# Performance work log

Measured on AMD Instinct MI355X. Metric: run time of the kernel, lower is better.

Reference implementation:

```python
import math
import jax, jax.numpy as jnp
import numpy as np

B, T, DIN, DH, E, TOPK = 2048, 512, 32, 96, 6, 2


def setup_inputs() -> dict:
    key = jax.random.key(0)
    ks = jax.random.split(key, 20)
    x = jax.random.normal(ks[0], (B, T, DIN), jnp.float32)
    lengths = jax.random.randint(ks[1], (B,), 1, T + 1)
    mask = (jnp.arange(T)[None, :] < lengths[:, None])

    def U(k, shape, fan):
        s = 1.0 / math.sqrt(fan)
        return jax.random.uniform(k, shape, jnp.float32, -s, s)

    # PyTorch LSTM init: U(-1/sqrt(DH), 1/sqrt(DH)); gate order i,f,g,o
    Wih = U(ks[2], (4 * DH, DIN), DH)
    Whh = U(ks[3], (4 * DH, DH), DH)
    bih = U(ks[4], (4 * DH,), DH)
    bhh = U(ks[5], (4 * DH,), DH)
    Wq = U(ks[6], (DH, DH), DH); bq = U(ks[7], (DH,), DH)
    Wk = U(ks[8], (DH, DH), DH); bk = U(ks[9], (DH,), DH)
    Wv = U(ks[10], (DH, DH), DH); bv = U(ks[11], (DH,), DH)
    Wg = U(ks[12], (E, 2 * DH), 2 * DH); bg = U(ks[13], (E,), 2 * DH)
    We1 = U(ks[14], (E, DH, 2 * DH), 2 * DH); be1 = U(ks[15], (E, DH), 2 * DH)
    We2 = U(ks[16], (E, DH), DH); be2 = U(ks[17], (E,), DH)
    return dict(x=x, lengths=lengths, mask=mask, Wih=Wih, Whh=Whh, bih=bih, bhh=bhh,
                Wq=Wq, bq=bq, Wk=Wk, bk=bk, Wv=Wv, bv=bv, Wg=Wg, bg=bg,
                We1=We1, be1=be1, We2=We2, be2=be2)


def _lstm(x, mask, Wih, Whh, bih, bhh):
    # packed-sequence semantics: carry frozen past each sample's length,
    # padded output positions zeroed (like pad_packed_sequence).
    xg = x @ Wih.T + bih  # [B,T,4*DH] precomputed input projection
    dh = Whh.shape[1]

    def step(carry, inp):
        h, c = carry
        xg_t, m_t = inp
        g = xg_t + h @ Whh.T + bhh
        i, f, gg, o = jnp.split(g, 4, axis=-1)
        c_new = jax.nn.sigmoid(f) * c + jax.nn.sigmoid(i) * jnp.tanh(gg)
        h_new = jax.nn.sigmoid(o) * jnp.tanh(c_new)
        m = m_t[:, None]
        h = jnp.where(m, h_new, h)
        c = jnp.where(m, c_new, c)
        return (h, c), jnp.where(m, h_new, 0.0)

    init = (jnp.zeros((x.shape[0], dh), x.dtype), jnp.zeros((x.shape[0], dh), x.dtype))
    (hT, _), H = jax.lax.scan(step, init, (jnp.swapaxes(xg, 0, 1), mask.T))
    return jnp.swapaxes(H, 0, 1), hT  # H:[B,T,DH], hT:[B,DH]


def reference(x, lengths, mask, Wih, Whh, bih, bhh, Wq, bq, Wk, bk, Wv, bv,
              Wg, bg, We1, be1, We2, be2):
    H, hT = _lstm(x, mask, Wih, Whh, bih, bhh)
    Q = hT @ Wq.T + bq                      # [B,DH]
    K = H @ Wk.T + bk                       # [B,T,DH]
    V = H @ Wv.T + bv                       # [B,T,DH]
    logits = jnp.einsum('bd,btd->bt', Q, K) / math.sqrt(K.shape[-1])
    logits = jnp.where(mask, logits, -1e9)
    alpha = jax.nn.softmax(logits, axis=1)  # [B,T]
    ctx = jnp.einsum('bt,btd->bd', alpha, V)
    feats = jnp.concatenate([ctx, hT], axis=-1)  # [B,2*DH]
    gate_logits = feats @ Wg.T + bg              # [B,E]
    topv, topi = jax.lax.top_k(gate_logits, TOPK)
    pi = jax.nn.softmax(topv, axis=-1)           # [B,TOPK]
    # all-expert dense compute (E tiny), then gather selected -> same math as
    # the per-expert masked scatter loop in the torch module (dropout off).
    h1 = jax.nn.relu(jnp.einsum('bf,ehf->beh', feats, We1) + be1[None])  # [B,E,DH]
    outs = jnp.einsum('beh,eh->be', h1, We2) + be2[None]                  # [B,E]
    sel = jnp.take_along_axis(outs, topi, axis=1)                         # [B,TOPK]
    yhat = jnp.sum(pi * sel, axis=-1, keepdims=True)                      # [B,1]
    return yhat, alpha, gate_logits
```

## Files before the change

kernel.cpp:

```cpp
#include <hip/hip_runtime.h>
#include <hip/hip_bf16.h>

#define B_ 2048
#define T_ 512
#define DIN_ 32
#define DH_ 96
#define NG_ 384
#define E_ 6

#define BPB 8
#define HP 104
#define GS 10

typedef __attribute__((ext_vector_type(8))) _Float16 f16x8;
typedef __attribute__((ext_vector_type(4))) float f32x4;

#if defined(__has_builtin)
# if __has_builtin(__builtin_amdgcn_exp2f)
#  define EXP2F(x) __builtin_amdgcn_exp2f(x)
# endif
# if __has_builtin(__builtin_amdgcn_rcpf)
#  define RCPF(x) __builtin_amdgcn_rcpf(x)
# endif
#endif
#ifndef EXP2F
# define EXP2F(x) exp2f(x)
#endif
#ifndef RCPF
# define RCPF(x) (1.0f/(x))
#endif

__device__ __forceinline__ float sigf(float x) {
    return RCPF(1.0f + EXP2F(x * -1.44269504f));
}
__device__ __forceinline__ float tanhf_(float x) {
    return 1.0f - 2.0f * RCPF(1.0f + EXP2F(x * 2.88539008f));
}

__device__ __forceinline__ f16x8 cvt8(float4 a, float4 b) {
    f16x8 r;
    r[0] = (_Float16)a.x; r[1] = (_Float16)a.y; r[2] = (_Float16)a.z; r[3] = (_Float16)a.w;
    r[4] = (_Float16)b.x; r[5] = (_Float16)b.y; r[6] = (_Float16)b.z; r[7] = (_Float16)b.w;
    return r;
}
__device__ __forceinline__ f16x8 cvt8p(const float* p) {
    return cvt8(*(const float4*)p, *(const float4*)(p + 4));
}

__device__ __forceinline__ void lds_barrier() {
    asm volatile("s_waitcnt lgkmcnt(0)\n\ts_barrier" ::: "memory");
}

__global__ __launch_bounds__(512) void sort_kernel(
    const int* __restrict__ lengths, int* __restrict__ perm) {
    __shared__ int sbins[512];
    __shared__ int soffs[512];
    const int tid = threadIdx.x;
    sbins[tid] = 0;
    __syncthreads();
    for (int b = tid; b < B_; b += 512) atomicAdd(&sbins[lengths[b] - 1], 1);
    __syncthreads();
    soffs[tid] = sbins[tid];
    __syncthreads();
    for (int d = 1; d < 512; d <<= 1) {
        int v = (tid >= d) ? soffs[tid - d] : 0;
        __syncthreads();
        soffs[tid] += v;
        __syncthreads();
    }
    int excl = soffs[tid] - sbins[tid];
    __syncthreads();
    soffs[tid] = excl;
    __syncthreads();
    for (int b = tid; b < B_; b += 512) {
        const int pos = atomicAdd(&soffs[lengths[b] - 1], 1);
        perm[pos] = b;
    }
}

__global__ __launch_bounds__(768, 1) void lstm_attn_kernel(
    const float* __restrict__ x, const int* __restrict__ lengths,
    const int* __restrict__ perm,
    const float* __restrict__ Wih, const float* __restrict__ Whh,
    const float* __restrict__ bih, const float* __restrict__ bhh,
    const float* __restrict__ Wq, const float* __restrict__ bq,
    const float* __restrict__ Wk, const float* __restrict__ bk,
    const float* __restrict__ Wv, const float* __restrict__ bv,
    const float* __restrict__ Wg, const float* __restrict__ bg,
    const float* __restrict__ We1, const float* __restrict__ be1,
    const float* __restrict__ We2, const float* __restrict__ be2,
    _Float16* __restrict__ Hout,
    float* __restrict__ yhat_out, float* __restrict__ alpha_out,
    float* __restrict__ gl_out)
{
    __shared__ float sgate[NG_ * GS];
    __shared__ _Float16 sh[2][8 * HP];
    __shared__ int sgb[BPB], slen[BPB];
    __shared__ float slog[BPB][T_];
    __shared__ float shT8[BPB][DH_];
    __shared__ float sQ8[BPB][DH_];
    __shared__ float sqk8[BPB][DH_];
    __shared__ float scraw[BPB][DH_];
    __shared__ float sfeats[BPB][2 * DH_];
    __shared__ float sh1_[BPB][2][DH_];
    __shared__ float sqb[BPB];
    __shared__ float sgl[BPB][E_];
    __shared__ float spi2[BPB][2];
    __shared__ float souts[BPB][2];
    __shared__ int stopi2[BPB][2];

    const int tid  = threadIdx.x;
    const int bb   = blockIdx.x * BPB;
    const int wave = tid >> 6;
    const int lane = tid & 63;
    const int col  = lane & 15;
    const int quad = lane >> 4;

    if (tid < BPB) {
        const int g = perm[bb + tid];
        sgb[tid] = g;
        slen[tid] = lengths[g];
    }
    {
        _Float16* shf = &sh[0][0];
        for (int i = tid; i < 2 * 8 * HP; i += 768) shf[i] = (_Float16)0.f;
    }
    __syncthreads();

    int bmax = slen[0];
#pragma unroll
    for (int i = 1; i < BPB; ++i) bmax = max(bmax, slen[i]);

    int gc[2]; float bias[2];
    f16x8 wh[2][3], wi[2];
#pragma unroll
    for (int j = 0; j < 2; ++j) {
        const int tau = wave * 2 + j;
        const int g = tau / 6, u6 = tau % 6;
        const int gcj = g * DH_ + u6 * 16 + col;
        gc[j] = gcj;
#pragma unroll
        for (int kf = 0; kf < 3; ++kf)
            wh[j][kf] = cvt8p(Whh + gcj * DH_ + kf * 32 + quad * 8);
        wi[j] = cvt8p(Wih + gcj * DIN_ + quad * 8);
        bias[j] = bih[gcj] + bhh[gcj];
    }

    const int eu = tid >> 3;
    const int eb = tid & 7;
    float c1 = 0.f, hk1 = 0.f;
    const int len1 = slen[eb];

    const bool st_act = tid < 384;
    const int sb = tid / 48;
    const int su = (tid % 48) * 2;
    _Float16* Hst = Hout + ((long long)sgb[sb] * T_) * DH_ + su;

    const bool arow = col < 8;
    const float* xp = x + ((long long)sgb[col & 7] * T_) * DIN_ + quad * 8;
    float4 xc0 = make_float4(0.f, 0.f, 0.f, 0.f), xc1 = xc0;
    if (arow) { xc0 = *(const float4*)xp; xc1 = *(const float4*)(xp + 4); }

    for (int t = 0; t < bmax; ++t) {
        const int buf = t & 1;

        f16x8 h0 = 0, h1 = 0, h2 = 0;
        if (arow) {
            const _Float16* hrow = &sh[buf][col * HP];
            h0 = *(const f16x8*)(hrow + 0  + quad * 8);
            h1 = *(const f16x8*)(hrow + 32 + quad * 8);
            h2 = *(const f16x8*)(hrow + 64 + quad * 8);
        }

        const float* xpn = (t + 1 < T_) ? (xp + DIN_) : xp;
        float4 xn0 = make_float4(0.f, 0.f, 0.f, 0.f), xn1 = xn0;
        if (arow) { xn0 = *(const float4*)xpn; xn1 = *(const float4*)(xpn + 4); }

        f16x8 xa = cvt8(xc0, xc1);

#pragma unroll
        for (int j = 0; j < 2; ++j) {
            f32x4 a = {bias[j], bias[j], bias[j], bias[j]};
            a = __builtin_amdgcn_mfma_f32_16x16x32_f16(h0, wh[j][0], a, 0, 0, 0);
            a = __builtin_amdgcn_mfma_f32_16x16x32_f16(h1, wh[j][1], a, 0, 0, 0);
            a = __builtin_amdgcn_mfma_f32_16x16x32_f16(h2, wh[j][2], a, 0, 0, 0);
            a = __builtin_amdgcn_mfma_f32_16x16x32_f16(xa, wi[j],    a, 0, 0, 0);
            if (quad < 2) {
                float2* sp = (float2*)&sgate[gc[j] * GS + quad * 4];
                sp[0] = float2{a[0], a[1]};
                sp[1] = float2{a[2], a[3]};
            }
        }
        lds_barrier();

        if (t > 0 && st_act) {
            unsigned v = *(const unsigned*)&sh[buf][sb * HP + su];
            *(unsigned*)Hst = v;
            Hst += DH_;
        }

        {
            float iv = sgate[(0 * DH_ + eu) * GS + eb];
            float fv = sgate[(1 * DH_ + eu) * GS + eb];
            float gv = sgate[(2 * DH_ + eu) * GS + eb];
            float ov = sgate[(3 * DH_ + eu) * GS + eb];
            float cn = sigf(fv) * c1 + sigf(iv) * tanhf_(gv);
            float hn = sigf(ov) * tanhf_(cn);
            const bool m = t < len1;
            c1  = m ? cn : c1;
            hk1 = m ? hn : hk1;
            sh[buf ^ 1][eb * HP + eu] = (_Float16)hk1;
        }
        lds_barrier();

        xp = xpn; xc0 = xn0; xc1 = xn1;
    }

    if (st_act) {
        unsigned v = *(const unsigned*)&sh[bmax & 1][sb * HP + su];
        *(unsigned*)Hst = v;
    }

    shT8[eb][eu] = hk1;
    __threadfence_block();
    __syncthreads();

    const int abi = tid / 96;
    const int au  = tid - abi * 96;
    const int ag  = sgb[abi];
    const int alen = slen[abi];
    const float scale = 0.10206207262f;

    {
        float acc = bq[au];
        const float* wr = Wq + au * DH_;
        const float* ht = &shT8[abi][0];
        for (int d = 0; d < DH_; d += 4) {
            float4 w4 = *(const float4*)(wr + d);
            acc += w4.x * ht[d] + w4.y * ht[d + 1] + w4.z * ht[d + 2] + w4.w * ht[d + 3];
        }
        sQ8[abi][au] = acc;
    }
    __syncthreads();

    {
        float acc = 0.f;
        const float* qv = &sQ8[abi][0];
        for (int j = 0; j < DH_; ++j) acc += Wk[j * DH_ + au] * qv[j];
        sqk8[abi][au] = acc * scale;
    }
    if (wave < 8) {
        float p = sQ8[wave][lane] * bk[lane];
        if (lane < 32) p += sQ8[wave][64 + lane] * bk[64 + lane];
        for (int off = 32; off; off >>= 1) p += __shfl_xor(p, off);
        if (lane == 0) sqb[wave] = p * scale;
    }
    __syncthreads();

    for (int k = 0; k < 6; ++k) {
        const int r = tid + k * 768;
        if (r < BPB * T_) {
            const int bi2 = r >> 9, t = r & (T_ - 1);
            float l = -1e30f;
            if (t < slen[bi2]) {
                const _Float16* hr = Hout + ((long long)sgb[bi2] * T_ + t) * DH_;
                const float* qk = &sqk8[bi2][0];
                float acc = sqb[bi2];
#pragma unroll
                for (int u = 0; u < DH_; u += 8) {
                    f16x8 hv = *(const f16x8*)(hr + u);
                    float4 qa = *(const float4*)(qk + u);
                    float4 qc = *(const float4*)(qk + u + 4);
                    acc += (float)hv[0] * qa.x + (float)hv[1] * qa.y
                         + (float)hv[2] * qa.z + (float)hv[3] * qa.w
                         + (float)hv[4] * qc.x + (float)hv[5] * qc.y
                         + (float)hv[6] * qc.z + (float)hv[7] * qc.w;
                }
                l = acc;
            }
            slog[0][r] = l;
        }
    }
    __syncthreads();

    if (wave < 8) {
        float lv[8];
#pragma unroll
        for (int j = 0; j < 8; ++j) lv[j] = slog[wave][lane + 64 * j];
        float m = lv[0];
#pragma unroll
        for (int j = 1; j < 8; ++j) m = fmaxf(m, lv[j]);
        for (int off = 32; off; off >>= 1) m = fmaxf(m, __shfl_xor(m, off));
        float ev[8]; float s = 0.f;
#pragma unroll
        for (int j = 0; j < 8; ++j) { ev[j] = EXP2F((lv[j] - m) * 1.44269504f); s += ev[j]; }
        for (int off = 32; off; off >>= 1) s += __shfl_xor(s, off);
        const float rinv = RCPF(s);
        float* aout = alpha_out + (long long)sgb[wave] * T_;
#pragma unroll
        for (int j = 0; j < 8; ++j) {
            const float a = ev[j] * rinv;
            slog[wave][lane + 64 * j] = a;
            aout[lane + 64 * j] = a;
        }
    }
    __syncthreads();

    {
        const int ub = au >> 3, tl = au & 7;
        float acc[8] = {0.f, 0.f, 0.f, 0.f, 0.f, 0.f, 0.f, 0.f};
        const _Float16* hb = Hout + ((long long)ag * T_) * DH_ + ub * 8;
        for (int k = 0; k < 64; ++k) {
            const int t = tl + (k << 3);
            if (t < alen) {
                f16x8 hv = *(const f16x8*)(hb + t * DH_);
                const float a = slog[abi][t];
#pragma unroll
                for (int i = 0; i < 8; ++i) acc[i] += a * (float)hv[i];
            }
        }
#pragma unroll
        for (int i = 0; i < 8; ++i) {
            acc[i] += __shfl_xor(acc[i], 1);
            acc[i] += __shfl_xor(acc[i], 2);
            acc[i] += __shfl_xor(acc[i], 4);
        }
        if (tl == 0) {
#pragma unroll
            for (int i = 0; i < 8; ++i) scraw[abi][ub * 8 + i] = acc[i];
        }
    }
    __syncthreads();

    {
        float acc = bv[au];
        const float* wr = Wv + au * DH_;
        const float* cr = &scraw[abi][0];
        for (int u2 = 0; u2 < DH_; u2 += 4) {
            float4 w4 = *(const float4*)(wr + u2);
            acc += w4.x * cr[u2] + w4.y * cr[u2 + 1] + w4.z * cr[u2 + 2] + w4.w * cr[u2 + 3];
        }
        sfeats[abi][au] = acc;
        sfeats[abi][DH_ + au] = shT8[abi][au];
    }
    __syncthreads();

    {
        const int ge = au >> 4, gcc = au & 15;
        float p = 0.f;
        const float* wg = Wg + ge * 2 * DH_ + gcc * 12;
        const float* ft = &sfeats[abi][gcc * 12];
#pragma unroll
        for (int j = 0; j < 12; ++j) p += wg[j] * ft[j];
        p += __shfl_xor(p, 1); p += __shfl_xor(p, 2);
        p += __shfl_xor(p, 4); p += __shfl_xor(p, 8);
        if (gcc == 0) {
            const float g2 = p + bg[ge];
            sgl[abi][ge] = g2;
            gl_out[ag * E_ + ge] = g2;
        }
    }
    __syncthreads();

    if (tid < BPB) {
        int i0 = 0; float v0 = sgl[tid][0];
        for (int ee = 1; ee < E_; ++ee) if (sgl[tid][ee] > v0) { v0 = sgl[tid][ee]; i0 = ee; }
        int i1 = -1; float v1 = -1e30f;
        for (int ee = 0; ee < E_; ++ee) {
            if (ee == i0) continue;
            if (sgl[tid][ee] > v1) { v1 = sgl[tid][ee]; i1 = ee; }
        }
        const float ex1 = EXP2F((v1 - v0) * 1.44269504f);
        const float inv = RCPF(1.f + ex1);
        spi2[tid][0] = inv; spi2[tid][1] = ex1 * inv;
        stopi2[tid][0] = i0; stopi2[tid][1] = i1;
    }
    __syncthreads();

#pragma unroll
    for (int e2 = 0; e2 < 2; ++e2) {
        const int ex = stopi2[abi][e2];
        float acc = be1[ex * DH_ + au];
        const float* w = We1 + ((long long)ex * DH_ + au) * (2 * DH_);
        const float* ft = &sfeats[abi][0];
        for (int f = 0; f < 2 * DH_; f += 4) {
            float4 w4 = *(const float4*)(w + f);
            acc += w4.x * ft[f] + w4.y * ft[f + 1] + w4.z * ft[f + 2] + w4.w * ft[f + 3];
        }
        sh1_[abi][e2][au] = fmaxf(acc, 0.f);
    }
    __syncthreads();

    if (wave < 8) {
        const int e2 = lane >> 5, lu = lane & 31;
        const int ex = stopi2[wave][e2];
        const float* w2 = We2 + ex * DH_;
        const float* h1p = &sh1_[wave][e2][0];
        float p = h1p[lu] * w2[lu] + h1p[lu + 32] * w2[lu + 32] + h1p[lu + 64] * w2[lu + 64];
        p += __shfl_xor(p, 1); p += __shfl_xor(p, 2); p += __shfl_xor(p, 4);
        p += __shfl_xor(p, 8); p += __shfl_xor(p, 16);
        if (lu == 0) souts[wave][e2] = p + be2[ex];
    }
    __syncthreads();
    if (tid < BPB)
        yhat_out[sgb[tid]] = spi2[tid][0] * souts[tid][0] + spi2[tid][1] * souts[tid][1];
}

extern "C" void kernel_launch(void* const* d_in, const int* in_sizes, int n_in,
                              void* d_out, int out_size, void* d_ws, size_t ws_size,
                              hipStream_t stream) {
    const float* x   = (const float*)d_in[0];
    const int* lengths = (const int*)d_in[1];
    const float* Wih = (const float*)d_in[3];
    const float* Whh = (const float*)d_in[4];
    const float* bih = (const float*)d_in[5];
    const float* bhh = (const float*)d_in[6];
    const float* Wq  = (const float*)d_in[7];
    const float* bq  = (const float*)d_in[8];
    const float* Wk  = (const float*)d_in[9];
    const float* bk  = (const float*)d_in[10];
    const float* Wv  = (const float*)d_in[11];
    const float* bv  = (const float*)d_in[12];
    const float* Wg  = (const float*)d_in[13];
    const float* bg  = (const float*)d_in[14];
    const float* We1 = (const float*)d_in[15];
    const float* be1 = (const float*)d_in[16];
    const float* We2 = (const float*)d_in[17];
    const float* be2 = (const float*)d_in[18];

    float* yhat  = (float*)d_out;
    float* alpha = yhat + B_;
    float* gl    = alpha + (size_t)B_ * T_;

    char* ws = (char*)d_ws;
    _Float16* Hws = (_Float16*)ws;
    int* perm   = (int*)(ws + (size_t)B_ * T_ * DH_ * 2);

    sort_kernel<<<dim3(1), dim3(512), 0, stream>>>(lengths, perm);

    lstm_attn_kernel<<<dim3(B_ / BPB), dim3(768), 0, stream>>>(
        x, lengths, perm, Wih, Whh, bih, bhh,
        Wq, bq, Wk, bk, Wv, bv, Wg, bg, We1, be1, We2, be2,
        Hws, yhat, alpha, gl);
}
```

Baseline: 718.6 us.

## Offload attention and MoE tail for long-sequence groups to a separate per-sample kernel

LSTM blocks whose longest sequence exceeds a threshold now write the final hidden state to workspace and exit early, skipping the in-kernel attention and MoE epilogue. A new kernel with one block per sample then does attention, gating and experts for those groups. This shortens the critical-path blocks, which already run the longest recurrences, and spreads their epilogue across many small blocks. The cost is an extra launch, a round trip of hT through global memory, and a re-read of H.

```diff
diff --git a/kernel.cpp b/kernel.cpp
--- a/kernel.cpp
+++ b/kernel.cpp
@@ -11,6 +11,7 @@
 #define BPB 8
 #define HP 104
 #define GS 10
+#define ATH 384
 
 typedef __attribute__((ext_vector_type(8))) _Float16 f16x8;
 typedef __attribute__((ext_vector_type(4))) float f32x4;
@@ -89,7 +90,7 @@
     const float* __restrict__ Wg, const float* __restrict__ bg,
     const float* __restrict__ We1, const float* __restrict__ be1,
     const float* __restrict__ We2, const float* __restrict__ be2,
-    _Float16* __restrict__ Hout,
+    _Float16* __restrict__ Hout, float* __restrict__ hT,
     float* __restrict__ yhat_out, float* __restrict__ alpha_out,
     float* __restrict__ gl_out)
 {
@@ -221,6 +222,10 @@
         *(unsigned*)Hst = v;
     }
 
+    hT[sgb[eb] * DH_ + eu] = hk1;
+
+    if (bmax > ATH) return;
+
     shT8[eb][eu] = hk1;
     __threadfence_block();
     __syncthreads();
@@ -404,6 +409,212 @@
     __syncthreads();
     if (tid < BPB)
         yhat_out[sgb[tid]] = spi2[tid][0] * souts[tid][0] + spi2[tid][1] * souts[tid][1];
+}
+
+__global__ __launch_bounds__(256) void attn_moe_kernel(
+    const _Float16* __restrict__ H, const float* __restrict__ hT,
+    const int* __restrict__ lengths, const int* __restrict__ perm,
+    const float* __restrict__ Wq, const float* __restrict__ bq,
+    const float* __restrict__ Wk, const float* __restrict__ bk,
+    const float* __restrict__ Wv, const float* __restrict__ bv,
+    const float* __restrict__ Wg, const float* __restrict__ bg,
+    const float* __restrict__ We1, const float* __restrict__ be1,
+    const float* __restrict__ We2, const float* __restrict__ be2,
+    float* __restrict__ yhat_out, float* __restrict__ alpha_out,
+    float* __restrict__ gl_out)
+{
+    const int p = blockIdx.x;
+    int gbm = 0;
+#pragma unroll
+    for (int k = 0; k < BPB; ++k)
+        gbm = max(gbm, lengths[perm[(p & ~(BPB - 1)) + k]]);
+    if (gbm <= ATH) return;
+
+    __shared__ float salpha[T_];
+    __shared__ float shT[DH_];
+    __shared__ float sQ[DH_];
+    __shared__ float sqk[DH_];
+    __shared__ float spart[DH_];
+    __shared__ float sfeats[2 * DH_];
+    __shared__ float sh1[2][DH_];
+    __shared__ float sred[4], ssum[4];
+    __shared__ float sgl[E_];
+    __shared__ float spi[2];
+    __shared__ float souts[2];
+    __shared__ float sqb_s;
+    __shared__ int stopi[2];
+
+    const int b = perm[p];
+    const int tid = threadIdx.x;
+    const int len = lengths[b];
+    const float scale = 0.10206207262f;
+
+    if (tid < DH_) shT[tid] = hT[b * DH_ + tid];
+    __syncthreads();
+    if (tid < DH_) {
+        float acc = bq[tid];
+        const float* wr = Wq + tid * DH_;
+        for (int d = 0; d < DH_; d += 4) {
+            float4 w4 = *(const float4*)(wr + d);
+            acc += w4.x * shT[d] + w4.y * shT[d + 1] + w4.z * shT[d + 2] + w4.w * shT[d + 3];
+        }
+        sQ[tid] = acc;
+    }
+    __syncthreads();
+    if (tid < DH_) {
+        float acc = 0.f;
+        for (int j = 0; j < DH_; ++j) acc += Wk[j * DH_ + tid] * sQ[j];
+        sqk[tid] = acc * scale;
+    }
+    if (tid >= 192) {
+        const int ln = tid - 192;
+        float pq = sQ[ln] * bk[ln];
+        if (ln < DH_ - 64) pq += sQ[ln + 64] * bk[ln + 64];
+        for (int off = 32; off; off >>= 1) pq += __shfl_xor(pq, off);
+        if (ln == 0) sqb_s = pq * scale;
+    }
+    __syncthreads();
+    const float qbv = sqb_s;
+
+    float lg[2]; bool vd[2];
+#pragma unroll
+    for (int hh = 0; hh < 2; ++hh) {
+        const int t = tid + hh * 256;
+        vd[hh] = t < len;
+        float l = qbv;
+        if (vd[hh]) {
+            const _Float16* hr = H + ((long long)b * T_ + t) * DH_;
+#pragma unroll
+            for (int u = 0; u < DH_; u += 8) {
+                f16x8 hv = *(const f16x8*)(hr + u);
+                float4 qa = *(const float4*)&sqk[u];
+                float4 qc = *(const float4*)&sqk[u + 4];
+                l += (float)hv[0] * qa.x + (float)hv[1] * qa.y
+                   + (float)hv[2] * qa.z + (float)hv[3] * qa.w
+                   + (float)hv[4] * qc.x + (float)hv[5] * qc.y
+                   + (float)hv[6] * qc.z + (float)hv[7] * qc.w;
+            }
+        }
+        lg[hh] = l;
+    }
+
+    float m = fmaxf(vd[0] ? lg[0] : -1e30f, vd[1] ? lg[1] : -1e30f);
+    for (int off = 32; off; off >>= 1) m = fmaxf(m, __shfl_xor(m, off));
+    if ((tid & 63) == 0) sred[tid >> 6] = m;
+    __syncthreads();
+    m = fmaxf(fmaxf(sred[0], sred[1]), fmaxf(sred[2], sred[3]));
+
+    float e0 = vd[0] ? EXP2F((lg[0] - m) * 1.44269504f) : 0.f;
+    float e1 = vd[1] ? EXP2F((lg[1] - m) * 1.44269504f) : 0.f;
+    float s = e0 + e1;
+    for (int off = 32; off; off >>= 1) s += __shfl_xor(s, off);
+    if ((tid & 63) == 0) ssum[tid >> 6] = s;
+    __syncthreads();
+    s = (ssum[0] + ssum[1]) + (ssum[2] + ssum[3]);
+
+    const float rinv = RCPF(s);
+    const float a0 = e0 * rinv, a1 = e1 * rinv;
+    salpha[tid] = a0;
+    salpha[tid + 256] = a1;
+    alpha_out[(long long)b * T_ + tid] = a0;
+    alpha_out[(long long)b * T_ + tid + 256] = a1;
+    __syncthreads();
+
+    if (tid < 192) {
+        const int ub = tid >> 4, tl = tid & 15;
+        float acc[8] = {0.f, 0.f, 0.f, 0.f, 0.f, 0.f, 0.f, 0.f};
+        const _Float16* hb = H + ((long long)b * T_) * DH_ + ub * 8;
+#pragma unroll 4
+        for (int k = 0; k < 32; ++k) {
+            const int t = tl + (k << 4);
+            if (t < len) {
+                f16x8 hv = *(const f16x8*)(hb + t * DH_);
+                const float a = salpha[t];
+#pragma unroll
+                for (int i = 0; i < 8; ++i) acc[i] += a * (float)hv[i];
+            }
+        }
+#pragma unroll
+        for (int i = 0; i < 8; ++i) {
+            acc[i] += __shfl_xor(acc[i], 1);
+            acc[i] += __shfl_xor(acc[i], 2);
+            acc[i] += __shfl_xor(acc[i], 4);
+            acc[i] += __shfl_xor(acc[i], 8);
+        }
+        if (tl == 0) {
+#pragma unroll
+            for (int i = 0; i < 8; ++i) spart[ub * 8 + i] = acc[i];
+        }
+    }
+    __syncthreads();
+
+    if (tid < DH_) {
+        float acc = bv[tid];
+        const float* wr = Wv + tid * DH_;
+        for (int u = 0; u < DH_; u += 4) {
+            float4 w4 = *(const float4*)(wr + u);
+            acc += w4.x * spart[u] + w4.y * spart[u + 1] + w4.z * spart[u + 2] + w4.w * spart[u + 3];
+        }
+        sfeats[tid] = acc;
+        sfeats[DH_ + tid] = shT[tid];
+    }
+    __syncthreads();
+
+    if (tid < 192) {
+        const int e6 = tid >> 5, cc = tid & 31;
+        float pq = 0.f;
+        const float* wg = Wg + e6 * 2 * DH_;
+#pragma unroll
+        for (int j = 0; j < 6; ++j) pq += wg[cc * 6 + j] * sfeats[cc * 6 + j];
+        for (int off = 16; off; off >>= 1) pq += __shfl_xor(pq, off);
+        if (cc == 0) {
+            float g = pq + bg[e6];
+            sgl[e6] = g;
+            gl_out[b * E_ + e6] = g;
+        }
+    }
+    __syncthreads();
+
+    if (tid == 0) {
+        int i0 = 0; float v0 = sgl[0];
+        for (int ee = 1; ee < E_; ++ee) if (sgl[ee] > v0) { v0 = sgl[ee]; i0 = ee; }
+        int i1 = -1; float v1 = -1e30f;
+        for (int ee = 0; ee < E_; ++ee) {
+            if (ee == i0) continue;
+            if (sgl[ee] > v1) { v1 = sgl[ee]; i1 = ee; }
+        }
+        float ex1 = EXP2F((v1 - v0) * 1.44269504f);
+        float inv = RCPF(1.f + ex1);
+        spi[0] = inv; spi[1] = ex1 * inv;
+        stopi[0] = i0; stopi[1] = i1;
+    }
+    __syncthreads();
+
+    if (tid < 192) {
+        const int e2 = tid / DH_, u = tid - e2 * DH_;
+        const int ex = stopi[e2];
+        float acc = be1[ex * DH_ + u];
+        const float* w = We1 + ((long long)ex * DH_ + u) * (2 * DH_);
+        for (int f = 0; f < 2 * DH_; f += 4) {
+            float4 w4 = *(const float4*)(w + f);
+            acc += w4.x * sfeats[f] + w4.y * sfeats[f + 1] + w4.z * sfeats[f + 2] + w4.w * sfeats[f + 3];
+        }
+        sh1[e2][u] = fmaxf(acc, 0.f);
+    }
+    __syncthreads();
+
+    if (tid < 128) {
+        const int e2 = tid >> 6, ln = tid & 63;
+        const int ex = stopi[e2];
+        const float* w2 = We2 + ex * DH_;
+        float pq = sh1[e2][ln] * w2[ln];
+        if (ln < DH_ - 64) pq += sh1[e2][ln + 64] * w2[ln + 64];
+        for (int off = 32; off; off >>= 1) pq += __shfl_xor(pq, off);
+        if (ln == 0) souts[e2] = pq + be2[ex];
+    }
+    __syncthreads();
+    if (tid == 0)
+        yhat_out[b] = spi[0] * souts[0] + spi[1] * souts[1];
 }
 
 extern "C" void kernel_launch(void* const* d_in, const int* in_sizes, int n_in,
@@ -434,12 +645,17 @@
 
     char* ws = (char*)d_ws;
     _Float16* Hws = (_Float16*)ws;
-    int* perm   = (int*)(ws + (size_t)B_ * T_ * DH_ * 2);
+    float* hTws = (float*)(ws + (size_t)B_ * T_ * DH_ * 2);
+    int* perm   = (int*)(hTws + (size_t)B_ * DH_);
 
     sort_kernel<<<dim3(1), dim3(512), 0, stream>>>(lengths, perm);
 
     lstm_attn_kernel<<<dim3(B_ / BPB), dim3(768), 0, stream>>>(
         x, lengths, perm, Wih, Whh, bih, bhh,
         Wq, bq, Wk, bk, Wv, bv, Wg, bg, We1, be1, We2, be2,
-        Hws, yhat, alpha, gl);
-}
+        Hws, hTws, yhat, alpha, gl);
+
+    attn_moe_kernel<<<dim3(B_), dim3(256), 0, stream>>>(
+        Hws, hTws, lengths, perm, Wq, bq, Wk, bk, Wv, bv, Wg, bg,
+        We1, be1, We2, be2, yhat, alpha, gl);
+}
```

After: 669.0 us. 1.07x faster.
